# Optimization experiments

Hardware: AMD Instinct MI355X
Metric: run time of the kernel (lower is better)

The kernel has to match this reference:

```python
import jax, jax.numpy as jnp
import numpy as np

N_ADAPTERS = 16
RANK = 16
ALPHA = 16.0
SCALING = ALPHA / RANK
B, S, IN, OUT = 32, 512, 1024, 4096


def setup_inputs() -> dict:
    key = jax.random.key(0)
    k1, k2, k3, k4, k5, k6 = jax.random.split(key, 6)
    hidden_states = jax.random.normal(k1, (B, S, IN), dtype=jnp.float32)
    adapter_ids = jax.random.randint(k2, (B,), 0, N_ADAPTERS, dtype=jnp.int64)
    W = jax.random.normal(k3, (IN, OUT), dtype=jnp.float32) * 0.02
    b = jax.random.normal(k4, (OUT,), dtype=jnp.float32) * 0.02
    lora_a = jax.random.normal(k5, (N_ADAPTERS, IN, RANK), dtype=jnp.float32) * (1.0 / np.sqrt(IN))
    lora_b = jax.random.normal(k6, (N_ADAPTERS, RANK, OUT), dtype=jnp.float32) * 0.02
    return {"hidden_states": hidden_states, "adapter_ids": adapter_ids,
            "W": W, "b": b, "lora_a": lora_a, "lora_b": lora_b}


def reference(hidden_states, adapter_ids, W, b, lora_a, lora_b):
    # Base Conv1D (GPT-2 style): x @ W + b  -> [B, S, OUT]
    base_output = jnp.einsum('bsi,io->bso', hidden_states, W) + b
    # Per-sample adapter gather (replaces the unique-id loop + boolean masks):
    a_sel = lora_a[adapter_ids]          # [B, IN, R]
    b_sel = lora_b[adapter_ids]          # [B, R, OUT]
    low_rank = jnp.einsum('bsi,bir->bsr', hidden_states, a_sel)   # [B, S, R]
    delta = jnp.einsum('bsr,bro->bso', low_rank, b_sel) * SCALING # [B, S, OUT]
    return base_output + delta
```

## Files before the change

### kernel.cpp

```cpp
#include <hip/hip_runtime.h>

#define M_TOT 16384
#define N_TOT 4096
#define K_TOT 1024
#define R_LORA 16

#define BM 256
#define BN 256
#define BK 64
#define NSTEP 64

typedef __attribute__((ext_vector_type(8))) short bf16x8_t;
typedef __attribute__((ext_vector_type(4))) float f32x4_t;

__device__ __forceinline__ unsigned short f2bf(float f) {
  unsigned u = __builtin_bit_cast(unsigned, f);
  u += 0x7FFFu + ((u >> 16) & 1u);
  return (unsigned short)(u >> 16);
}

__device__ __forceinline__ void gload_lds16(const void* g, void* l) {
  __builtin_amdgcn_global_load_lds(
      (const __attribute__((address_space(1))) unsigned int*)g,
      (__attribute__((address_space(3))) unsigned int*)l, 16, 0, 0);
}

__global__ __launch_bounds__(256) void prep_kernel(const float* __restrict__ x,
                                                   const float* __restrict__ W,
                                                   const float* __restrict__ lora_a,
                                                   const float* __restrict__ lora_b,
                                                   unsigned short* __restrict__ xB,
                                                   unsigned short* __restrict__ WtB,
                                                   unsigned short* __restrict__ AtB,
                                                   unsigned short* __restrict__ lbT) {
  __shared__ float lds[64][65];
  const int bid = blockIdx.x;
  const int t = threadIdx.x;
  if (bid < 1024) {
    size_t i = (size_t)bid * 256 + t;
    const size_t stride = (size_t)1024 * 256;
    const size_t n4 = (size_t)M_TOT * K_TOT / 4;
    for (; i < n4; i += stride) {
      float4 v = ((const float4*)x)[i];
      ushort4 h;
      h.x = f2bf(v.x); h.y = f2bf(v.y); h.z = f2bf(v.z); h.w = f2bf(v.w);
      ((ushort4*)xB)[i] = h;
    }
  } else if (bid < 2048) {
    const int v = bid - 1024;
    const int k0 = (v & 15) * 64;
    const int n0 = (v >> 4) * 64;
    const int rr = t >> 4;
    const int cc = (t & 15) * 4;
#pragma unroll
    for (int i = 0; i < 4; ++i) {
      int row = i * 16 + rr;
      float4 w4 = *(const float4*)(W + (size_t)(k0 + row) * N_TOT + n0 + cc);
      lds[row][cc + 0] = w4.x; lds[row][cc + 1] = w4.y;
      lds[row][cc + 2] = w4.z; lds[row][cc + 3] = w4.w;
    }
    __syncthreads();
#pragma unroll
    for (int i = 0; i < 4; ++i) {
      int nrow = i * 16 + rr;
      ushort4 h;
      h.x = f2bf(lds[cc + 0][nrow]); h.y = f2bf(lds[cc + 1][nrow]);
      h.z = f2bf(lds[cc + 2][nrow]); h.w = f2bf(lds[cc + 3][nrow]);
      *(ushort4*)(WtB + (size_t)(n0 + nrow) * K_TOT + k0 + cc) = h;
    }
  } else {
    const int b2 = bid - 2048;
    if (b2 < 64) {
      int idx = b2 * 256 + t;
      int aid = idx >> 10;
      int k = idx & 1023;
      const float* src = lora_a + (size_t)idx * 16;
#pragma unroll
      for (int q = 0; q < 4; ++q) {
        float4 v4 = ((const float4*)src)[q];
#pragma unroll
        for (int j = 0; j < 4; ++j) {
          int r = q * 4 + j;
          float val = (j == 0) ? v4.x : (j == 1) ? v4.y : (j == 2) ? v4.z : v4.w;
          AtB[(((size_t)aid * 16 + r) << 10) + k] = f2bf(val);
        }
      }
    } else {
      int idx = (b2 - 64) * 256 + t;
      int aid = idx >> 12;
      int n = idx & 4095;
      unsigned short o[16];
#pragma unroll
      for (int r = 0; r < 16; ++r)
        o[r] = f2bf(lora_b[((size_t)aid * 16 + r) * N_TOT + n]);
      ushort4* dst = (ushort4*)(lbT + ((size_t)aid * N_TOT + n) * 16);
#pragma unroll
      for (int q = 0; q < 4; ++q) {
        ushort4 h; h.x = o[q*4+0]; h.y = o[q*4+1]; h.z = o[q*4+2]; h.w = o[q*4+3];
        dst[q] = h;
      }
    }
  }
}

__global__ __launch_bounds__(256) void lowrank_kernel(const unsigned short* __restrict__ xB,
                                                      const unsigned short* __restrict__ AtB,
                                                      const int* __restrict__ aids,
                                                      unsigned short* __restrict__ lrB) {
  __shared__ char As[128 * 128];
  const int blk = blockIdx.x;
  const int t = threadIdx.x;
  const int lane = t & 63;
  const int w = t >> 6;
  const int fr = lane & 15, fq = lane >> 4;
  const int aid = aids[blk >> 2];

  const unsigned short* aSrc[4];
  char* aDst[4];
#pragma unroll
  for (int r = 0; r < 4; ++r) {
    int off = (r * 256 + t) * 16;
    int row = off >> 7, cb = off & 127;
    int sb = cb ^ ((row & 7) << 4);
    aSrc[r] = xB + (size_t)(blk * 128 + row) * K_TOT + (sb >> 1);
    aDst[r] = As + off;
  }
  const unsigned short* bBase = AtB + ((size_t)aid * 16 + fr) * K_TOT + fq * 8;

  f32x4_t acc[2];
  acc[0] = (f32x4_t){0.f, 0.f, 0.f, 0.f};
  acc[1] = (f32x4_t){0.f, 0.f, 0.f, 0.f};

  for (int kt = 0; kt < K_TOT / 64; ++kt) {
#pragma unroll
    for (int r = 0; r < 4; ++r) gload_lds16(aSrc[r] + kt * 64, aDst[r]);
    __syncthreads();
#pragma unroll
    for (int ks = 0; ks < 2; ++ks) {
      bf16x8_t bfr = *(const bf16x8_t*)(bBase + kt * 64 + ks * 32);
#pragma unroll
      for (int m = 0; m < 2; ++m) {
        int row = w * 32 + m * 16 + fr;
        int cb = ks * 64 + fq * 16;
        bf16x8_t af = *(const bf16x8_t*)(As + row * 128 + (cb ^ ((row & 7) << 4)));
        acc[m] = __builtin_amdgcn_mfma_f32_16x16x32_bf16(af, bfr, acc[m], 0, 0, 0);
      }
    }
    __syncthreads();
  }
#pragma unroll
  for (int m = 0; m < 2; ++m) {
    int gm0 = blk * 128 + w * 32 + m * 16 + fq * 4;
#pragma unroll
    for (int q = 0; q < 4; ++q)
      lrB[(size_t)(gm0 + q) * R_LORA + fr] = f2bf(acc[m][q]);
  }
}

#define BAR() __builtin_amdgcn_s_barrier()
#define WAIT_LGKM0() asm volatile("s_waitcnt lgkmcnt(0)" ::: "memory")

#define STAGE_HALF(gbase, koff, ldsbase)                                   \
  do {                                                                     \
    gload_lds16((const char*)(gbase) + (koff), (ldsbase) + t * 16);        \
    gload_lds16((const char*)(gbase) + 64 * 2048 + (koff),                 \
                (ldsbase) + 8192 + t * 16);                                \
  } while (0)

#define LDA(MH)                                                            \
  do {                                                                     \
    _Pragma("unroll") for (int m = 0; m < 4; ++m)                          \
      _Pragma("unroll") for (int ks = 0; ks < 2; ++ks)                     \
        aF[m][ks] = *(const bf16x8_t*)(bufA + (MH) * 8192 + m * 2048 +     \
                                       (laneA ^ (ks << 6)));               \
  } while (0)

#define LDB(NH)                                                            \
  do {                                                                     \
    _Pragma("unroll") for (int n = 0; n < 2; ++n)                          \
      _Pragma("unroll") for (int ks = 0; ks < 2; ++ks)                     \
        bF[NH][n][ks] = *(const bf16x8_t*)(bufB + (NH) * 4096 + n * 2048 + \
                                           (laneA ^ (ks << 6)));           \
  } while (0)

#define MM(MH, NH)                                                         \
  do {                                                                     \
    __builtin_amdgcn_s_setprio(1);                                         \
    _Pragma("unroll") for (int ks = 0; ks < 2; ++ks)                       \
      _Pragma("unroll") for (int m = 0; m < 4; ++m)                        \
        _Pragma("unroll") for (int n = 0; n < 2; ++n)                      \
          acc[(MH) * 4 + m][(NH) * 2 + n] =                                \
              __builtin_amdgcn_mfma_f32_16x16x32_bf16(                     \
                  aF[m][ks], bF[NH][n][ks],                                \
                  acc[(MH) * 4 + m][(NH) * 2 + n], 0, 0, 0);               \
    __builtin_amdgcn_s_setprio(0);                                         \
  } while (0)

__global__ __launch_bounds__(512, 2) void gemm_kernel(
    const unsigned short* __restrict__ xB, const unsigned short* __restrict__ WtB,
    const unsigned short* __restrict__ lrB, const unsigned short* __restrict__ lbT,
    const float* __restrict__ bias, const int* __restrict__ aids,
    float* __restrict__ out) {
  __shared__ char smem[131072];

  const int orig = blockIdx.x;
  const int xcd = orig & 7;
  const int j = orig >> 3;
  const int tn = xcd * 2 + (j & 1);
  const int tmg = j >> 1;

  const int t = threadIdx.x;
  const int lane = t & 63;
  const int wid = t >> 6;
  const int wr = wid >> 2;
  const int wc = wid & 3;
  const int fr = lane & 15, fq = lane >> 4;

  const int laneA = fr * 128 + (((fq << 4) ^ ((fr & 7) << 4)));
  const int waveAoff = wr * 16384;
  const int waveBoff = 32768 + (wc >> 1) * 16384 + (wc & 1) * 8192;

  const int srow = t >> 3;
  const int sb = (((t & 7) ^ (srow & 7)) << 4);
  const char* pAbase = (const char*)xB + (size_t)(tmg * 1024 + srow) * 2048 + sb;
  const char* pBpanel = (const char*)WtB + (size_t)(tn * 256 + srow) * 2048 + sb;

  f32x4_t acc[8][4];
#pragma unroll
  for (int m = 0; m < 8; ++m)
#pragma unroll
    for (int n = 0; n < 4; ++n) acc[m][n] = (f32x4_t){0.f, 0.f, 0.f, 0.f};

  bf16x8_t aF[4][2];
  bf16x8_t bF[2][2][2];

  STAGE_HALF(pAbase, 0, smem + 0);
  STAGE_HALF(pAbase + (size_t)128 * 2048, 0, smem + 16384);
  STAGE_HALF(pBpanel, 0, smem + 32768);
  STAGE_HALF(pBpanel + (size_t)128 * 2048, 0, smem + 49152);
  STAGE_HALF(pBpanel, 128, smem + 65536 + 32768);
  STAGE_HALF(pBpanel + (size_t)128 * 2048, 128, smem + 65536 + 49152);
  asm volatile("s_waitcnt vmcnt(4)" ::: "memory");
  BAR();

#pragma unroll 1
  for (int s = 0; s < NSTEP; ++s) {
    char* base = smem + ((s & 1) << 16);
    char* nbase = smem + (((s + 1) & 1) << 16);
    char* bufA = base + waveAoff;
    char* bufB = base + waveBoff;

    const int u1 = s + 1;
    const bool stA = (u1 < NSTEP);
    const char* pA1 = pAbase + (size_t)(u1 >> 4) * (256 * 2048);
    const int ka1 = (u1 & 15) * 128;

    const int u2 = s + 2;
    const bool stB = (u2 < NSTEP);
    const int kb2 = (u2 & 15) * 128;

    LDA(0);
    LDB(0);
    if (stA) STAGE_HALF(pA1, ka1, nbase + 0);
    asm volatile("s_waitcnt lgkmcnt(8)" ::: "memory");
    BAR(); WAIT_LGKM0();
    MM(0, 0);
    BAR();

    LDB(1);
    if (stA) STAGE_HALF(pA1 + (size_t)128 * 2048, ka1, nbase + 16384);
    BAR(); WAIT_LGKM0();
    MM(0, 1);
    BAR();

    LDA(1);
    if (stB) STAGE_HALF(pBpanel, kb2, base + 32768);
    BAR(); WAIT_LGKM0();
    MM(1, 1);
    BAR();

    if (stB) STAGE_HALF(pBpanel + (size_t)128 * 2048, kb2, base + 49152);
    BAR(); WAIT_LGKM0();
    MM(1, 0);
    if (s < NSTEP - 2) asm volatile("s_waitcnt vmcnt(4)" ::: "memory");
    else               asm volatile("s_waitcnt vmcnt(0)" ::: "memory");
    BAR();

    if ((s & 15) == 15) {
      const int tm = tmg * 4 + (s >> 4);
      const int aid = aids[tm >> 1];
      bf16x8_t z8 = (bf16x8_t){0, 0, 0, 0, 0, 0, 0, 0};
      bf16x8_t lrf[8], lbf[4];
#pragma unroll
      for (int m = 0; m < 8; ++m) lrf[m] = z8;
#pragma unroll
      for (int n = 0; n < 4; ++n) lbf[n] = z8;
      if (fq < 2) {
#pragma unroll
        for (int m = 0; m < 8; ++m)
          lrf[m] = *(const bf16x8_t*)(lrB + (size_t)(tm * 256 + wr * 128 + m * 16 + fr) * R_LORA + fq * 8);
#pragma unroll
        for (int n = 0; n < 4; ++n)
          lbf[n] = *(const bf16x8_t*)(lbT + ((size_t)aid * N_TOT + tn * 256 + wc * 64 + n * 16 + fr) * R_LORA + fq * 8);
      }
#pragma unroll
      for (int m = 0; m < 8; ++m)
#pragma unroll
        for (int n = 0; n < 4; ++n)
          acc[m][n] = __builtin_amdgcn_mfma_f32_16x16x32_bf16(lrf[m], lbf[n], acc[m][n], 0, 0, 0);

#pragma unroll
      for (int n = 0; n < 4; ++n) {
        int gn = tn * 256 + wc * 64 + n * 16 + fr;
        float bv = bias[gn];
#pragma unroll
        for (int m = 0; m < 8; ++m) {
          int gm0 = tm * 256 + wr * 128 + m * 16 + fq * 4;
          float* op = out + (size_t)gm0 * N_TOT + gn;
#pragma unroll
          for (int q = 0; q < 4; ++q) op[(size_t)q * N_TOT] = acc[m][n][q] + bv;
        }
      }
#pragma unroll
      for (int m = 0; m < 8; ++m)
#pragma unroll
        for (int n = 0; n < 4; ++n) acc[m][n] = (f32x4_t){0.f, 0.f, 0.f, 0.f};
    }
  }
}

extern "C" void kernel_launch(void* const* d_in, const int* in_sizes, int n_in,
                              void* d_out, int out_size, void* d_ws, size_t ws_size,
                              hipStream_t stream) {
  const float* x      = (const float*)d_in[0];
  const int*   aids   = (const int*)d_in[1];
  const float* W      = (const float*)d_in[2];
  const float* bias   = (const float*)d_in[3];
  const float* lora_a = (const float*)d_in[4];
  const float* lora_b = (const float*)d_in[5];
  float* out = (float*)d_out;

  char* ws = (char*)d_ws;
  unsigned short* xB  = (unsigned short*)(ws);
  unsigned short* WtB = (unsigned short*)(ws + (size_t)32 * 1024 * 1024);
  unsigned short* lrB = (unsigned short*)(ws + (size_t)40 * 1024 * 1024);
  unsigned short* AtB = (unsigned short*)(ws + (size_t)40 * 1024 * 1024 + 512 * 1024);
  unsigned short* lbT = (unsigned short*)(ws + (size_t)41 * 1024 * 1024);

  prep_kernel<<<2368, 256, 0, stream>>>(x, W, lora_a, lora_b, xB, WtB, AtB, lbT);
  lowrank_kernel<<<128, 256, 0, stream>>>(xB, AtB, aids, lrB);
  gemm_kernel<<<256, 512, 0, stream>>>(xB, WtB, lrB, lbT, bias, aids, out);
}
```

Measured before the change: 214.5 us.

## Replace ping-pong staged LDS pipeline with simple double-buffered load-all-then-compute loop

Replaces the fine-grained four-phase schedule (interleaved LDS fragment loads, staged global-to-LDS copies for A one step ahead and B two steps ahead, with barriers between MFMA quarters) with a plain double buffer. Each iteration now issues all next-step A and B loads up front, reads all fragments, runs the four MFMA blocks, and ends with a single __syncthreads. This cuts the barrier count and simplifies the code. It gives up the intra-iteration overlap and prioritized MFMA interleaving, and holds more fragment registers live at once, which may pressure the two-blocks-per-CU occupancy target.

Result: faster. 207.6 us (-3.2%).

```diff
diff --git a/kernel.cpp b/kernel.cpp
--- a/kernel.cpp
+++ b/kernel.cpp
@@ -157,9 +157,6 @@
   }
 }
 
-#define BAR() __builtin_amdgcn_s_barrier()
-#define WAIT_LGKM0() asm volatile("s_waitcnt lgkmcnt(0)" ::: "memory")
-
 #define STAGE_HALF(gbase, koff, ldsbase)                                   \
   do {                                                                     \
     gload_lds16((const char*)(gbase) + (koff), (ldsbase) + t * 16);        \
@@ -167,23 +164,7 @@
                 (ldsbase) + 8192 + t * 16);                                \
   } while (0)
 
-#define LDA(MH)                                                            \
-  do {                                                                     \
-    _Pragma("unroll") for (int m = 0; m < 4; ++m)                          \
-      _Pragma("unroll") for (int ks = 0; ks < 2; ++ks)                     \
-        aF[m][ks] = *(const bf16x8_t*)(bufA + (MH) * 8192 + m * 2048 +     \
-                                       (laneA ^ (ks << 6)));               \
-  } while (0)
-
-#define LDB(NH)                                                            \
-  do {                                                                     \
-    _Pragma("unroll") for (int n = 0; n < 2; ++n)                          \
-      _Pragma("unroll") for (int ks = 0; ks < 2; ++ks)                     \
-        bF[NH][n][ks] = *(const bf16x8_t*)(bufB + (NH) * 4096 + n * 2048 + \
-                                           (laneA ^ (ks << 6)));           \
-  } while (0)
-
-#define MM(MH, NH)                                                         \
+#define MM(AS, BS, MH, NH)                                                 \
   do {                                                                     \
     __builtin_amdgcn_s_setprio(1);                                         \
     _Pragma("unroll") for (int ks = 0; ks < 2; ++ks)                       \
@@ -191,7 +172,7 @@
         _Pragma("unroll") for (int n = 0; n < 2; ++n)                      \
           acc[(MH) * 4 + m][(NH) * 2 + n] =                                \
               __builtin_amdgcn_mfma_f32_16x16x32_bf16(                     \
-                  aF[m][ks], bF[NH][n][ks],                                \
+                  AS[m][ks], BS[n][ks],                                    \
                   acc[(MH) * 4 + m][(NH) * 2 + n], 0, 0, 0);               \
     __builtin_amdgcn_s_setprio(0);                                         \
   } while (0)
@@ -231,17 +212,11 @@
 #pragma unroll
     for (int n = 0; n < 4; ++n) acc[m][n] = (f32x4_t){0.f, 0.f, 0.f, 0.f};
 
-  bf16x8_t aF[4][2];
-  bf16x8_t bF[2][2][2];
-
   STAGE_HALF(pAbase, 0, smem + 0);
   STAGE_HALF(pAbase + (size_t)128 * 2048, 0, smem + 16384);
   STAGE_HALF(pBpanel, 0, smem + 32768);
   STAGE_HALF(pBpanel + (size_t)128 * 2048, 0, smem + 49152);
-  STAGE_HALF(pBpanel, 128, smem + 65536 + 32768);
-  STAGE_HALF(pBpanel + (size_t)128 * 2048, 128, smem + 65536 + 49152);
-  asm volatile("s_waitcnt vmcnt(4)" ::: "memory");
-  BAR();
+  __syncthreads();
 
 #pragma unroll 1
   for (int s = 0; s < NSTEP; ++s) {
@@ -251,40 +226,41 @@
     char* bufB = base + waveBoff;
 
     const int u1 = s + 1;
-    const bool stA = (u1 < NSTEP);
-    const char* pA1 = pAbase + (size_t)(u1 >> 4) * (256 * 2048);
-    const int ka1 = (u1 & 15) * 128;
-
-    const int u2 = s + 2;
-    const bool stB = (u2 < NSTEP);
-    const int kb2 = (u2 & 15) * 128;
-
-    LDA(0);
-    LDB(0);
-    if (stA) STAGE_HALF(pA1, ka1, nbase + 0);
-    asm volatile("s_waitcnt lgkmcnt(8)" ::: "memory");
-    BAR(); WAIT_LGKM0();
-    MM(0, 0);
-    BAR();
-
-    LDB(1);
-    if (stA) STAGE_HALF(pA1 + (size_t)128 * 2048, ka1, nbase + 16384);
-    BAR(); WAIT_LGKM0();
-    MM(0, 1);
-    BAR();
-
-    LDA(1);
-    if (stB) STAGE_HALF(pBpanel, kb2, base + 32768);
-    BAR(); WAIT_LGKM0();
-    MM(1, 1);
-    BAR();
-
-    if (stB) STAGE_HALF(pBpanel + (size_t)128 * 2048, kb2, base + 49152);
-    BAR(); WAIT_LGKM0();
-    MM(1, 0);
-    if (s < NSTEP - 2) asm volatile("s_waitcnt vmcnt(4)" ::: "memory");
-    else               asm volatile("s_waitcnt vmcnt(0)" ::: "memory");
-    BAR();
+    if (u1 < NSTEP) {
+      const char* pA1 = pAbase + (size_t)(u1 >> 4) * (256 * 2048);
+      const int k1 = (u1 & 15) * 128;
+      STAGE_HALF(pA1, k1, nbase + 0);
+      STAGE_HALF(pA1 + (size_t)128 * 2048, k1, nbase + 16384);
+      STAGE_HALF(pBpanel, k1, nbase + 32768);
+      STAGE_HALF(pBpanel + (size_t)128 * 2048, k1, nbase + 49152);
+    }
+
+    bf16x8_t a0F[4][2], a1F[4][2], b0F[2][2], b1F[2][2];
+#pragma unroll
+    for (int n = 0; n < 2; ++n)
+#pragma unroll
+      for (int ks = 0; ks < 2; ++ks)
+        b0F[n][ks] = *(const bf16x8_t*)(bufB + n * 2048 + (laneA ^ (ks << 6)));
+#pragma unroll
+    for (int m = 0; m < 4; ++m)
+#pragma unroll
+      for (int ks = 0; ks < 2; ++ks)
+        a0F[m][ks] = *(const bf16x8_t*)(bufA + m * 2048 + (laneA ^ (ks << 6)));
+#pragma unroll
+    for (int n = 0; n < 2; ++n)
+#pragma unroll
+      for (int ks = 0; ks < 2; ++ks)
+        b1F[n][ks] = *(const bf16x8_t*)(bufB + 4096 + n * 2048 + (laneA ^ (ks << 6)));
+#pragma unroll
+    for (int m = 0; m < 4; ++m)
+#pragma unroll
+      for (int ks = 0; ks < 2; ++ks)
+        a1F[m][ks] = *(const bf16x8_t*)(bufA + 8192 + m * 2048 + (laneA ^ (ks << 6)));
+
+    MM(a0F, b0F, 0, 0);
+    MM(a0F, b1F, 0, 1);
+    MM(a1F, b1F, 1, 1);
+    MM(a1F, b0F, 1, 0);
 
     if ((s & 15) == 15) {
       const int tm = tmg * 4 + (s >> 4);
@@ -326,6 +302,8 @@
 #pragma unroll
         for (int n = 0; n < 4; ++n) acc[m][n] = (f32x4_t){0.f, 0.f, 0.f, 0.f};
     }
+
+    __syncthreads();
   }
 }
 
```
